# Performance work log

Hardware: AMD Instinct MI355X
Metric: run time of the kernel (lower is better)

## Reference

```python
import jax, jax.numpy as jnp
import numpy as np

N = 50000
NEG_SLOPE = 0.2

def gat_conv(x, src, dst, W, a_src, a_dst, bias, heads, out_ch):
    # Linear projection per head: [N, H, C]
    h = (x @ W).reshape(x.shape[0], heads, out_ch)
    # Node-level attention terms alpha_src/alpha_dst: [N, H]
    al_src = jnp.einsum('nhc,hc->nh', h, a_src)
    al_dst = jnp.einsum('nhc,hc->nh', h, a_dst)
    # Edge logits with LeakyReLU: [E, H]
    logits = jax.nn.leaky_relu(al_src[src] + al_dst[dst], NEG_SLOPE)
    # Segment softmax over incoming edges of each dst node
    m = jax.ops.segment_max(logits, dst, num_segments=N)
    e = jnp.exp(logits - m[dst])
    s = jax.ops.segment_sum(e, dst, num_segments=N)
    alpha = e / (s[dst] + 1e-16)                      # [E, H]
    # Weighted message aggregation (scatter-add): [N, H, C]
    out = jax.ops.segment_sum(h[src] * alpha[..., None], dst, num_segments=N)
    return out.reshape(N, heads * out_ch) + bias


def setup_inputs() -> dict:
    key = jax.random.key(0)
    ks = jax.random.split(key, 12)
    in_ch, out_ch = 128, 256
    h1, c1 = 4, out_ch // 8          # conv1: 4 heads x 32
    mid = h1 * c1                    # 128 = out_ch // 2
    E = 1600000
    x = jax.random.normal(ks[0], (N, in_ch), jnp.float32)
    edge_index = jax.random.randint(ks[1], (2, E), 0, N, jnp.int64)
    sc = 0.1
    return {
        'x': x,
        'edge_index': edge_index,
        'W1': jax.random.normal(ks[2], (in_ch, h1 * c1), jnp.float32) * sc,
        'a_src1': jax.random.normal(ks[3], (h1, c1), jnp.float32) * sc,
        'a_dst1': jax.random.normal(ks[4], (h1, c1), jnp.float32) * sc,
        'b1': jnp.zeros((h1 * c1,), jnp.float32),
        'W2': jax.random.normal(ks[5], (mid, out_ch), jnp.float32) * sc,
        'a_src2': jax.random.normal(ks[6], (1, out_ch), jnp.float32) * sc,
        'a_dst2': jax.random.normal(ks[7], (1, out_ch), jnp.float32) * sc,
        'b2': jnp.zeros((out_ch,), jnp.float32),
    }


def reference(x, edge_index, W1, a_src1, a_dst1, b1, W2, a_src2, a_dst2, b2):
    # PyG GATConv adds self-loops by default
    loop = jnp.arange(N, dtype=edge_index.dtype)
    src = jnp.concatenate([edge_index[0], loop])
    dst = jnp.concatenate([edge_index[1], loop])
    h = gat_conv(x, src, dst, W1, a_src1, a_dst1, b1, heads=4, out_ch=32)
    h = jax.nn.relu(h)
    out = gat_conv(h, src, dst, W2, a_src2, a_dst2, b2, heads=1, out_ch=256)
    return out
```

## Files before the change

### kernel.cpp

```cpp
#include <hip/hip_runtime.h>
#include <hip/hip_fp16.h>
#include <math.h>

#define NSLOPE 0.2f
#define LOG2E  1.44269504f

typedef _Float16 half8 __attribute__((ext_vector_type(8)));
typedef float floatx4 __attribute__((ext_vector_type(4)));
typedef float floatx2 __attribute__((ext_vector_type(2)));

__device__ __forceinline__ float wcalc(float t) {
    float l = fmaxf(t, NSLOPE * t);
    float r;
    asm("v_exp_f32 %0, %1" : "=v"(r) : "v"(l));
    return r;
}

__device__ __forceinline__ void fma_mix8(float* acc, float w, const uint4& v) {
    const unsigned* u = reinterpret_cast<const unsigned*>(&v);
#pragma unroll
    for (int i = 0; i < 4; ++i) {
        asm("v_fma_mix_f32 %0, %1, %2, %0 op_sel:[0,0,0] op_sel_hi:[1,0,0]"
            : "+v"(acc[2 * i]) : "v"(u[i]), "v"(w));
        asm("v_fma_mix_f32 %0, %1, %2, %0 op_sel:[1,0,0] op_sel_hi:[1,0,0]"
            : "+v"(acc[2 * i + 1]) : "v"(u[i]), "v"(w));
    }
}

__device__ __forceinline__ void fma8_fp8(float* acc, float w, uint2 v) {
    floatx2 p0 = __builtin_amdgcn_cvt_pk_f32_fp8(v.x, false);
    floatx2 p1 = __builtin_amdgcn_cvt_pk_f32_fp8(v.x, true);
    floatx2 p2 = __builtin_amdgcn_cvt_pk_f32_fp8(v.y, false);
    floatx2 p3 = __builtin_amdgcn_cvt_pk_f32_fp8(v.y, true);
    acc[0] = fmaf(w, p0.x, acc[0]);
    acc[1] = fmaf(w, p0.y, acc[1]);
    acc[2] = fmaf(w, p1.x, acc[2]);
    acc[3] = fmaf(w, p1.y, acc[3]);
    acc[4] = fmaf(w, p2.x, acc[4]);
    acc[5] = fmaf(w, p2.y, acc[5]);
    acc[6] = fmaf(w, p3.x, acc[6]);
    acc[7] = fmaf(w, p3.y, acc[7]);
}

#define MAXB 5632
#define BE   8192

__global__ __launch_bounds__(256)
void prep_kernel(const int* __restrict__ dst, int* __restrict__ bcnt,
                 const float* __restrict__ x, __half* __restrict__ x16, int nx,
                 const float* __restrict__ W1, __half* __restrict__ W1T,
                 const float* __restrict__ W2, __half* __restrict__ W2T,
                 const float* __restrict__ a_src2, const float* __restrict__ a_dst2,
                 float* __restrict__ w2s, float* __restrict__ w2d,
                 int E, int Etot, int nb, int nbA, int ncast, int nt1, int nt2)
{
    __shared__ int hist[512];
    int bid = blockIdx.x;
    int tid = threadIdx.x;

    if (bid < nbA) {
        for (int i = tid; i < 512; i += 256) hist[i] = 0;
        __syncthreads();
        for (int e = bid * 256 + tid; e < Etot; e += nbA * 256) {
            int d = (e < E) ? dst[e] : (e - E);
            atomicAdd(&hist[d >> 7], 1);
        }
        __syncthreads();
        for (int i = tid; i < nb; i += 256) {
            int v = hist[i];
            if (v) atomicAdd(&bcnt[i], v);
        }
        return;
    }
    bid -= nbA;
    if (bid < ncast) {
        int i = (bid * 256 + tid) * 4;
        if (i < nx) {
            float4 v = *(const float4*)&x[i];
            __half2 a = __floats2half2_rn(v.x, v.y);
            __half2 b = __floats2half2_rn(v.z, v.w);
            *(uint2*)&x16[i] = make_uint2(*(unsigned*)&a, *(unsigned*)&b);
        }
        return;
    }
    bid -= ncast;
    if (bid < nt1) {
        int idx = bid * 256 + tid;
        int c = idx >> 7, k = idx & 127;
        W1T[(size_t)c * 128 + k] = __float2half(W1[(size_t)k * 128 + c]);
        return;
    }
    bid -= nt1;
    if (bid < nt2) {
        int idx = bid * 256 + tid;
        int c = idx >> 7, k = idx & 127;
        W2T[(size_t)c * 128 + k] = __float2half(W2[(size_t)k * 256 + c]);
        return;
    }
    {
        const float* a = (tid < 128) ? a_src2 : a_dst2;
        int k = tid & 127;
        float acc = 0.f;
        for (int c = 0; c < 256; c += 4) {
            float4 w = *(const float4*)&W2[(size_t)k * 256 + c];
            float4 av = *(const float4*)&a[c];
            acc = fmaf(w.x, av.x, fmaf(w.y, av.y, fmaf(w.z, av.z, fmaf(w.w, av.w, acc))));
        }
        if (tid < 128) w2s[k] = acc * LOG2E; else w2d[k] = acc * LOG2E;
    }
}

__global__ __launch_bounds__(512)
void scanBuckets_kernel(const int* __restrict__ bcnt, int* __restrict__ bbase,
                        int* __restrict__ gcur, int nb, int* __restrict__ offs,
                        int N, int total)
{
    __shared__ int tmp[512];
    int tid = threadIdx.x;
    int v = (tid < nb) ? bcnt[tid] : 0;
    tmp[tid] = v;
    __syncthreads();
    for (int off = 1; off < 512; off <<= 1) {
        int t = (tid >= off) ? tmp[tid - off] : 0;
        __syncthreads();
        tmp[tid] += t;
        __syncthreads();
    }
    if (tid < nb) {
        int e = tmp[tid] - v;
        bbase[tid] = e;
        gcur[tid] = e;
    }
    if (tid == 0) offs[N] = total;
}

__global__ __launch_bounds__(256)
void bucketB_kernel(const int* __restrict__ src, const int* __restrict__ dst,
                    int* __restrict__ gcur, unsigned* __restrict__ eout,
                    int E, int Etot, int nb)
{
    __shared__ int hist[512];
    __shared__ int res[512];
    __shared__ int lcur[512];
    int tid = threadIdx.x;
    int e0 = blockIdx.x * BE;
    int e1 = min(e0 + BE, Etot);

    for (int i = tid; i < 512; i += 256) hist[i] = 0;
    __syncthreads();
    for (int e = e0 + tid; e < e1; e += 256) {
        int d = (e < E) ? dst[e] : (e - E);
        atomicAdd(&hist[d >> 7], 1);
    }
    __syncthreads();
    for (int i = tid; i < nb; i += 256) {
        int h = hist[i];
        res[i] = h ? atomicAdd(&gcur[i], h) : 0;
        lcur[i] = 0;
    }
    __syncthreads();
    for (int e = e0 + tid; e < e1; e += 256) {
        int s, d;
        if (e < E) { s = src[e]; d = dst[e]; }
        else       { s = e - E; d = s; }
        int b = d >> 7;
        int p = res[b] + atomicAdd(&lcur[b], 1);
        eout[p] = (unsigned)s | ((unsigned)(d & 127) << 16);
    }
}

__global__ __launch_bounds__(256)
void combo_kernel(const unsigned* __restrict__ eout, const int* __restrict__ bbase,
                  const int* __restrict__ bcnt, unsigned short* __restrict__ csr,
                  int* __restrict__ offs, int N, int nb,
                  const __half* __restrict__ A16, const __half* __restrict__ W1T,
                  const float* __restrict__ a_src, const float* __restrict__ a_dst,
                  unsigned char* __restrict__ h1, float* __restrict__ al_src,
                  float* __restrict__ al_dst)
{
    __shared__ unsigned eb[MAXB];
    __shared__ unsigned short sbuf[MAXB];
    __shared__ int cnt128[128], cur128[128], sc[128];

    int tid = threadIdx.x;
    if ((int)blockIdx.x < nb) {
        int b = blockIdx.x;
        int ebase = bbase[b];
        int ecnt = bcnt[b];
        int n0 = b << 7;
        int ncount = min(128, N - n0);

        if (tid < 128) cnt128[tid] = 0;
        for (int i = tid; i < ecnt; i += 256) eb[i] = eout[ebase + i];
        __syncthreads();
        for (int i = tid; i < ecnt; i += 256) atomicAdd(&cnt128[eb[i] >> 16], 1);
        __syncthreads();
        if (tid < 128) sc[tid] = cnt128[tid];
        __syncthreads();
        for (int off = 1; off < 128; off <<= 1) {
            int t = (tid >= off && tid < 128) ? sc[tid - off] : 0;
            __syncthreads();
            if (tid < 128) sc[tid] += t;
            __syncthreads();
        }
        if (tid < 128) {
            int excl = sc[tid] - cnt128[tid];
            cur128[tid] = excl;
            if (tid < ncount) offs[n0 + tid] = ebase + excl;
        }
        __syncthreads();
        for (int i = tid; i < ecnt; i += 256) {
            unsigned v = eb[i];
            int p = atomicAdd(&cur128[v >> 16], 1);
            sbuf[p] = (unsigned short)(v & 0xFFFFu);
        }
        __syncthreads();
        for (int i = tid; i < ecnt; i += 256) csr[ebase + i] = sbuf[i];
        return;
    }

    int gb = blockIdx.x - nb;
    int M = N;
    int wave = tid >> 6, lane = tid & 63;
    int lr = lane & 15, q = lane >> 4;
    int r0 = gb * 32 + (wave >> 1) * 16;
    int wcol = (wave & 1) * 64;

    int arow = min(r0 + lr, M - 1);
    const uint4* Arow = (const uint4*)A16 + (size_t)arow * 16;
    half8 a[4];
#pragma unroll
    for (int kb = 0; kb < 4; ++kb) {
        union { uint4 u; half8 h; } c;
        c.u = Arow[kb * 4 + q];
        a[kb] = c.h;
    }

    floatx4 acc[4];
    const floatx4 zero = {0.f, 0.f, 0.f, 0.f};
#pragma unroll
    for (int ct = 0; ct < 4; ++ct) acc[ct] = zero;

#pragma unroll
    for (int ct = 0; ct < 4; ++ct) {
        const uint4* Brow = (const uint4*)W1T + (size_t)(wcol + ct * 16 + lr) * 16;
#pragma unroll
        for (int kb = 0; kb < 4; ++kb) {
            union { uint4 u; half8 h; } c;
            c.u = Brow[kb * 4 + q];
            acc[ct] = __builtin_amdgcn_mfma_f32_16x16x32_f16(a[kb], c.h, acc[ct], 0, 0, 0);
        }
    }

#pragma unroll
    for (int ct = 0; ct < 4; ++ct) {
        int col = wcol + ct * 16 + lr;
#pragma unroll
        for (int r = 0; r < 4; ++r) {
            int row = r0 + q * 4 + r;
            if (row < M) {
                unsigned pk = __builtin_amdgcn_cvt_pk_fp8_f32(acc[ct][r], acc[ct][r], 0, false);
                h1[(size_t)row * 128 + col] = (unsigned char)(pk & 0xFF);
            }
        }
    }

    float as[4], ad[4];
#pragma unroll
    for (int ct = 0; ct < 4; ++ct) {
        int col = wcol + ct * 16 + lr;
        as[ct] = a_src[col] * LOG2E;
        ad[ct] = a_dst[col] * LOG2E;
    }
    int hb = wcol >> 5;
#pragma unroll
    for (int r = 0; r < 4; ++r) {
        float psA = acc[0][r] * as[0] + acc[1][r] * as[1];
        float psB = acc[2][r] * as[2] + acc[3][r] * as[3];
        float pdA = acc[0][r] * ad[0] + acc[1][r] * ad[1];
        float pdB = acc[2][r] * ad[2] + acc[3][r] * ad[3];
#pragma unroll
        for (int off = 1; off < 16; off <<= 1) {
            psA += __shfl_xor(psA, off); psB += __shfl_xor(psB, off);
            pdA += __shfl_xor(pdA, off); pdB += __shfl_xor(pdB, off);
        }
        if (lr == 0) {
            int row = r0 + q * 4 + r;
            if (row < M) {
                al_src[(size_t)row * 4 + hb]     = psA;
                al_src[(size_t)row * 4 + hb + 1] = psB;
                al_dst[(size_t)row * 4 + hb]     = pdA;
                al_dst[(size_t)row * 4 + hb + 1] = pdB;
            }
        }
    }
}

__global__ __launch_bounds__(256)
void gemm2_mfma(const __half* __restrict__ A16, const __half* __restrict__ W2T,
                const float* __restrict__ bias, float* __restrict__ out, int M)
{
    int wave = threadIdx.x >> 6, lane = threadIdx.x & 63;
    int lr = lane & 15, q = lane >> 4;
    int r0 = blockIdx.x * 16;
    int c0 = wave * 64;

    int arow = min(r0 + lr, M - 1);
    const uint4* Arow = (const uint4*)A16 + (size_t)arow * 16;
    half8 a[4];
#pragma unroll
    for (int kb = 0; kb < 4; ++kb) {
        union { uint4 u; half8 h; } c;
        c.u = Arow[kb * 4 + q];
        a[kb] = c.h;
    }

    floatx4 acc[4];
    const floatx4 zero = {0.f, 0.f, 0.f, 0.f};
#pragma unroll
    for (int ct = 0; ct < 4; ++ct) acc[ct] = zero;

#pragma unroll
    for (int ct = 0; ct < 4; ++ct) {
        const uint4* Brow = (const uint4*)W2T + (size_t)(c0 + ct * 16 + lr) * 16;
#pragma unroll
        for (int kb = 0; kb < 4; ++kb) {
            union { uint4 u; half8 h; } c;
            c.u = Brow[kb * 4 + q];
            acc[ct] = __builtin_amdgcn_mfma_f32_16x16x32_f16(a[kb], c.h, acc[ct], 0, 0, 0);
        }
    }

#pragma unroll
    for (int ct = 0; ct < 4; ++ct) {
        int col = c0 + ct * 16 + lr;
        float b = bias[col];
#pragma unroll
        for (int r = 0; r < 4; ++r) {
            int row = r0 + q * 4 + r;
            if (row < M) out[(size_t)row * 256 + col] = acc[ct][r] + b;
        }
    }
}

__global__ __launch_bounds__(256)
void agg1_kernel(const unsigned char* __restrict__ feat, const unsigned short* __restrict__ csr_src,
                 const int* __restrict__ offs, const float* __restrict__ alS,
                 const float* __restrict__ alD, const float* __restrict__ bias,
                 const float* __restrict__ w2s, const float* __restrict__ w2d,
                 __half* __restrict__ hmid, float* __restrict__ alS2,
                 float* __restrict__ alD2, int N)
{
    int lane = threadIdx.x & 63;
    int n = blockIdx.x * 4 + (threadIdx.x >> 6);
    if (n >= N) return;

    int lc = lane & 15;
    int es = lane >> 4;
    int h = lc >> 2;

    float aD = alD[(size_t)n * 4 + h];
    int beg = offs[n], end = offs[n + 1];

    float acc0[8] = {0,0,0,0,0,0,0,0}, acc1[8] = {0,0,0,0,0,0,0,0};
    float sw0 = 0.f, sw1 = 0.f;
    const char* fbase = (const char*)feat + lc * 8;
    const float* alSh = alS + h;

    int j = beg + es;
    for (; j + 12 < end; j += 16) {
        int s0 = csr_src[j];
        int s1 = csr_src[j + 4];
        int s2 = csr_src[j + 8];
        int s3 = csr_src[j + 12];
        float w0 = wcalc(alSh[(size_t)s0 * 4] + aD);
        float w1 = wcalc(alSh[(size_t)s1 * 4] + aD);
        float w2 = wcalc(alSh[(size_t)s2 * 4] + aD);
        float w3 = wcalc(alSh[(size_t)s3 * 4] + aD);
        uint2 f0 = *(const uint2*)(fbase + (size_t)s0 * 128);
        uint2 f1 = *(const uint2*)(fbase + (size_t)s1 * 128);
        uint2 f2 = *(const uint2*)(fbase + (size_t)s2 * 128);
        uint2 f3 = *(const uint2*)(fbase + (size_t)s3 * 128);
        fma8_fp8(acc0, w0, f0); sw0 += w0;
        fma8_fp8(acc1, w1, f1); sw1 += w1;
        fma8_fp8(acc0, w2, f2); sw0 += w2;
        fma8_fp8(acc1, w3, f3); sw1 += w3;
    }
    for (; j < end; j += 4) {
        int s0 = csr_src[j];
        float w0 = wcalc(alSh[(size_t)s0 * 4] + aD);
        uint2 f0 = *(const uint2*)(fbase + (size_t)s0 * 128);
        fma8_fp8(acc0, w0, f0); sw0 += w0;
    }

    float sw = sw0 + sw1;
    sw += __shfl_xor(sw, 16); sw += __shfl_xor(sw, 32);
#pragma unroll
    for (int i = 0; i < 8; ++i) {
        acc0[i] += acc1[i];
        acc0[i] += __shfl_xor(acc0[i], 16);
        acc0[i] += __shfl_xor(acc0[i], 32);
    }

    if (lane < 16) {
        float inv = 1.f / (sw + 1e-16f);
        float v[8];
#pragma unroll
        for (int i = 0; i < 8; ++i)
            v[i] = fmaxf(fmaf(acc0[i], inv, bias[lc * 8 + i]), 0.f);
        __half2 p0 = __floats2half2_rn(v[0], v[1]);
        __half2 p1 = __floats2half2_rn(v[2], v[3]);
        __half2 p2 = __floats2half2_rn(v[4], v[5]);
        __half2 p3 = __floats2half2_rn(v[6], v[7]);
        uint4 pk = make_uint4(*(unsigned*)&p0, *(unsigned*)&p1,
                              *(unsigned*)&p2, *(unsigned*)&p3);
        ((uint4*)hmid)[(size_t)n * 16 + lc] = pk;
        float ps = 0.f, pd = 0.f;
#pragma unroll
        for (int i = 0; i < 8; ++i) {
            ps = fmaf(v[i], w2s[lc * 8 + i], ps);
            pd = fmaf(v[i], w2d[lc * 8 + i], pd);
        }
        ps += __shfl_xor(ps, 1); ps += __shfl_xor(ps, 2);
        ps += __shfl_xor(ps, 4); ps += __shfl_xor(ps, 8);
        pd += __shfl_xor(pd, 1); pd += __shfl_xor(pd, 2);
        pd += __shfl_xor(pd, 4); pd += __shfl_xor(pd, 8);
        if (lane == 0) { alS2[n] = ps; alD2[n] = pd; }
    }
}

__global__ __launch_bounds__(256)
void agg2_kernel(const __half* __restrict__ feat, const unsigned short* __restrict__ csr_src,
                 const int* __restrict__ offs, const float* __restrict__ alS,
                 const float* __restrict__ alD, __half* __restrict__ m16, int N)
{
    int lane = threadIdx.x & 63;
    int n = blockIdx.x * 4 + (threadIdx.x >> 6);
    if (n >= N) return;

    int lc = lane & 15;
    int es = lane >> 4;

    float aD = alD[n];
    int beg = offs[n], end = offs[n + 1];

    float acc0[8] = {0,0,0,0,0,0,0,0}, acc1[8] = {0,0,0,0,0,0,0,0};
    float sw0 = 0.f, sw1 = 0.f;
    const char* fbase = (const char*)feat + lc * 16;

    int j = beg + es;
    for (; j + 12 < end; j += 16) {
        int s0 = csr_src[j];
        int s1 = csr_src[j + 4];
        int s2 = csr_src[j + 8];
        int s3 = csr_src[j + 12];
        float w0 = wcalc(alS[s0] + aD);
        float w1 = wcalc(alS[s1] + aD);
        float w2 = wcalc(alS[s2] + aD);
        float w3 = wcalc(alS[s3] + aD);
        uint4 f0 = *(const uint4*)(fbase + (size_t)s0 * 256);
        uint4 f1 = *(const uint4*)(fbase + (size_t)s1 * 256);
        uint4 f2 = *(const uint4*)(fbase + (size_t)s2 * 256);
        uint4 f3 = *(const uint4*)(fbase + (size_t)s3 * 256);
        fma_mix8(acc0, w0, f0); sw0 += w0;
        fma_mix8(acc1, w1, f1); sw1 += w1;
        fma_mix8(acc0, w2, f2); sw0 += w2;
        fma_mix8(acc1, w3, f3); sw1 += w3;
    }
    for (; j < end; j += 4) {
        int s0 = csr_src[j];
        float w0 = wcalc(alS[s0] + aD);
        uint4 f0 = *(const uint4*)(fbase + (size_t)s0 * 256);
        fma_mix8(acc0, w0, f0); sw0 += w0;
    }

    float sw = sw0 + sw1;
    sw += __shfl_xor(sw, 16); sw += __shfl_xor(sw, 32);
#pragma unroll
    for (int i = 0; i < 8; ++i) {
        acc0[i] += acc1[i];
        acc0[i] += __shfl_xor(acc0[i], 16);
        acc0[i] += __shfl_xor(acc0[i], 32);
    }

    if (lane < 16) {
        float inv = 1.f / (sw + 1e-16f);
        float v[8];
#pragma unroll
        for (int i = 0; i < 8; ++i) v[i] = acc0[i] * inv;
        __half2 p0 = __floats2half2_rn(v[0], v[1]);
        __half2 p1 = __floats2half2_rn(v[2], v[3]);
        __half2 p2 = __floats2half2_rn(v[4], v[5]);
        __half2 p3 = __floats2half2_rn(v[6], v[7]);
        uint4 pk = make_uint4(*(unsigned*)&p0, *(unsigned*)&p1,
                              *(unsigned*)&p2, *(unsigned*)&p3);
        ((uint4*)m16)[(size_t)n * 16 + lc] = pk;
    }
}

extern "C" void kernel_launch(void* const* d_in, const int* in_sizes, int n_in,
                              void* d_out, int out_size, void* d_ws, size_t ws_size,
                              hipStream_t stream)
{
    const float* x      = (const float*)d_in[0];
    const int*   ei     = (const int*)d_in[1];
    const float* W1     = (const float*)d_in[2];
    const float* a_src1 = (const float*)d_in[3];
    const float* a_dst1 = (const float*)d_in[4];
    const float* b1     = (const float*)d_in[5];
    const float* W2     = (const float*)d_in[6];
    const float* a_src2 = (const float*)d_in[7];
    const float* a_dst2 = (const float*)d_in[8];
    const float* b2     = (const float*)d_in[9];

    const int N    = in_sizes[0] / 128;
    const int E    = in_sizes[1] / 2;
    const int Etot = E + N;
    const int* src = ei;
    const int* dst = ei + E;
    const int nb   = (N + 127) >> 7;

    char* ws = (char*)d_ws;
    size_t off = 0;
    auto carve = [&](size_t bytes) -> void* {
        void* p = ws + off;
        off += (bytes + 255) & ~(size_t)255;
        return p;
    };
    __half*  x16  = (__half*)carve((size_t)N * 128 * 2);
    unsigned char* h1 = (unsigned char*)carve((size_t)N * 128);
    __half*  hmid = (__half*)carve((size_t)N * 128 * 2);
    __half*  m16  = (__half*)carve((size_t)N * 128 * 2);
    __half*  W1T  = (__half*)carve(128 * 128 * 2);
    __half*  W2T  = (__half*)carve(256 * 128 * 2);
    float*   alS1 = (float*)carve((size_t)N * 4 * 4);
    float*   alD1 = (float*)carve((size_t)N * 4 * 4);
    float*   alS2 = (float*)carve((size_t)N * 4);
    float*   alD2 = (float*)carve((size_t)N * 4);
    float*   w2s  = (float*)carve(128 * 4);
    float*   w2d  = (float*)carve(128 * 4);
    int*     offs = (int*)carve((size_t)(N + 1) * 4);
    int*     bcnt = (int*)carve(512 * 4);
    int*     bbas = (int*)carve(512 * 4);
    int*     gcur = (int*)carve(512 * 4);
    unsigned* eout = (unsigned*)carve((size_t)Etot * 4);
    unsigned short* csr = (unsigned short*)carve((size_t)Etot * 2);
    (void)ws_size; (void)n_in; (void)out_size;

    const int TB = 256;
    const int agrid = (N + 3) / 4;
    const int g1grid = (N + 31) / 32;
    const int g2grid = (N + 15) / 16;
    const int nx = N * 128;

    const int nbA   = 512;
    const int ncast = (nx / 4 + TB - 1) / TB;
    const int nt1   = (128 * 128 + TB - 1) / TB;
    const int nt2   = (256 * 128 + TB - 1) / TB;
    const int nprep = nbA + ncast + nt1 + nt2 + 1;

    hipMemsetAsync(bcnt, 0, 512 * 4, stream);

    prep_kernel<<<nprep, TB, 0, stream>>>(dst, bcnt, x, x16, nx, W1, W1T, W2, W2T,
                                          a_src2, a_dst2, w2s, w2d,
                                          E, Etot, nb, nbA, ncast, nt1, nt2);
    scanBuckets_kernel<<<1, 512, 0, stream>>>(bcnt, bbas, gcur, nb, offs, N, Etot);
    bucketB_kernel<<<(Etot + BE - 1) / BE, TB, 0, stream>>>(src, dst, gcur, eout, E, Etot, nb);
    combo_kernel<<<nb + g1grid, TB, 0, stream>>>(eout, bbas, bcnt, csr, offs, N, nb,
                                                 x16, W1T, a_src1, a_dst1, h1, alS1, alD1);
    agg1_kernel<<<agrid, TB, 0, stream>>>(h1, csr, offs, alS1, alD1, b1,
                                          w2s, w2d, hmid, alS2, alD2, N);
    agg2_kernel<<<agrid, TB, 0, stream>>>(hmid, csr, offs, alS2, alD2, m16, N);
    gemm2_mfma<<<g2grid, TB, 0, stream>>>(m16, W2T, b2, (float*)d_out, N);
}
```

Baseline: 299.7 us.

## Split feature aggregation into column halves with fp8 intermediates for cache locality

```diff
diff --git a/kernel.cpp b/kernel.cpp
--- a/kernel.cpp
+++ b/kernel.cpp
@@ -14,17 +14,6 @@
     float r;
     asm("v_exp_f32 %0, %1" : "=v"(r) : "v"(l));
     return r;
-}
-
-__device__ __forceinline__ void fma_mix8(float* acc, float w, const uint4& v) {
-    const unsigned* u = reinterpret_cast<const unsigned*>(&v);
-#pragma unroll
-    for (int i = 0; i < 4; ++i) {
-        asm("v_fma_mix_f32 %0, %1, %2, %0 op_sel:[0,0,0] op_sel_hi:[1,0,0]"
-            : "+v"(acc[2 * i]) : "v"(u[i]), "v"(w));
-        asm("v_fma_mix_f32 %0, %1, %2, %0 op_sel:[1,0,0] op_sel_hi:[1,0,0]"
-            : "+v"(acc[2 * i + 1]) : "v"(u[i]), "v"(w));
-    }
 }
 
 __device__ __forceinline__ void fma8_fp8(float* acc, float w, uint2 v) {
@@ -175,8 +164,8 @@
                   int* __restrict__ offs, int N, int nb,
                   const __half* __restrict__ A16, const __half* __restrict__ W1T,
                   const float* __restrict__ a_src, const float* __restrict__ a_dst,
-                  unsigned char* __restrict__ h1, float* __restrict__ al_src,
-                  float* __restrict__ al_dst)
+                  unsigned char* __restrict__ h1A, unsigned char* __restrict__ h1B,
+                  float* __restrict__ al_src, float* __restrict__ al_dst)
 {
     __shared__ unsigned eb[MAXB];
     __shared__ unsigned short sbuf[MAXB];
@@ -225,6 +214,7 @@
     int lr = lane & 15, q = lane >> 4;
     int r0 = gb * 32 + (wave >> 1) * 16;
     int wcol = (wave & 1) * 64;
+    unsigned char* hT = (wave & 1) ? h1B : h1A;
 
     int arow = min(r0 + lr, M - 1);
     const uint4* Arow = (const uint4*)A16 + (size_t)arow * 16;
@@ -254,13 +244,13 @@
 
 #pragma unroll
     for (int ct = 0; ct < 4; ++ct) {
-        int col = wcol + ct * 16 + lr;
+        int colh = ct * 16 + lr;
 #pragma unroll
         for (int r = 0; r < 4; ++r) {
             int row = r0 + q * 4 + r;
             if (row < M) {
                 unsigned pk = __builtin_amdgcn_cvt_pk_fp8_f32(acc[ct][r], acc[ct][r], 0, false);
-                h1[(size_t)row * 128 + col] = (unsigned char)(pk & 0xFF);
+                hT[(size_t)row * 64 + colh] = (unsigned char)(pk & 0xFF);
             }
         }
     }
@@ -344,146 +334,135 @@
 }
 
 __global__ __launch_bounds__(256)
-void agg1_kernel(const unsigned char* __restrict__ feat, const unsigned short* __restrict__ csr_src,
-                 const int* __restrict__ offs, const float* __restrict__ alS,
-                 const float* __restrict__ alD, const float* __restrict__ bias,
-                 const float* __restrict__ w2s, const float* __restrict__ w2d,
-                 __half* __restrict__ hmid, float* __restrict__ alS2,
-                 float* __restrict__ alD2, int N)
+void agg1_half_kernel(const unsigned char* __restrict__ feat,
+                      const unsigned short* __restrict__ csr_src,
+                      const int* __restrict__ offs, const float* __restrict__ alS,
+                      const float* __restrict__ alD, const float* __restrict__ bias,
+                      const float* __restrict__ w2s, const float* __restrict__ w2d,
+                      unsigned char* __restrict__ hmidH, float* __restrict__ alS2,
+                      float* __restrict__ alD2, int N, int half)
 {
     int lane = threadIdx.x & 63;
     int n = blockIdx.x * 4 + (threadIdx.x >> 6);
     if (n >= N) return;
 
-    int lc = lane & 15;
-    int es = lane >> 4;
-    int h = lc >> 2;
-
-    float aD = alD[(size_t)n * 4 + h];
+    int lc = lane & 7;
+    int es = lane >> 3;
+    int head = half * 2 + (lc >> 2);
+
+    float aD = alD[(size_t)n * 4 + head];
     int beg = offs[n], end = offs[n + 1];
 
     float acc0[8] = {0,0,0,0,0,0,0,0}, acc1[8] = {0,0,0,0,0,0,0,0};
     float sw0 = 0.f, sw1 = 0.f;
     const char* fbase = (const char*)feat + lc * 8;
-    const float* alSh = alS + h;
+    const float* alSh = alS + head;
 
     int j = beg + es;
-    for (; j + 12 < end; j += 16) {
+    for (; j + 8 < end; j += 16) {
         int s0 = csr_src[j];
-        int s1 = csr_src[j + 4];
-        int s2 = csr_src[j + 8];
-        int s3 = csr_src[j + 12];
+        int s1 = csr_src[j + 8];
         float w0 = wcalc(alSh[(size_t)s0 * 4] + aD);
         float w1 = wcalc(alSh[(size_t)s1 * 4] + aD);
-        float w2 = wcalc(alSh[(size_t)s2 * 4] + aD);
-        float w3 = wcalc(alSh[(size_t)s3 * 4] + aD);
-        uint2 f0 = *(const uint2*)(fbase + (size_t)s0 * 128);
-        uint2 f1 = *(const uint2*)(fbase + (size_t)s1 * 128);
-        uint2 f2 = *(const uint2*)(fbase + (size_t)s2 * 128);
-        uint2 f3 = *(const uint2*)(fbase + (size_t)s3 * 128);
+        uint2 f0 = *(const uint2*)(fbase + (size_t)s0 * 64);
+        uint2 f1 = *(const uint2*)(fbase + (size_t)s1 * 64);
         fma8_fp8(acc0, w0, f0); sw0 += w0;
         fma8_fp8(acc1, w1, f1); sw1 += w1;
-        fma8_fp8(acc0, w2, f2); sw0 += w2;
-        fma8_fp8(acc1, w3, f3); sw1 += w3;
-    }
-    for (; j < end; j += 4) {
+    }
+    if (j < end) {
         int s0 = csr_src[j];
         float w0 = wcalc(alSh[(size_t)s0 * 4] + aD);
-        uint2 f0 = *(const uint2*)(fbase + (size_t)s0 * 128);
+        uint2 f0 = *(const uint2*)(fbase + (size_t)s0 * 64);
         fma8_fp8(acc0, w0, f0); sw0 += w0;
     }
 
     float sw = sw0 + sw1;
-    sw += __shfl_xor(sw, 16); sw += __shfl_xor(sw, 32);
+    sw += __shfl_xor(sw, 8); sw += __shfl_xor(sw, 16); sw += __shfl_xor(sw, 32);
 #pragma unroll
     for (int i = 0; i < 8; ++i) {
         acc0[i] += acc1[i];
+        acc0[i] += __shfl_xor(acc0[i], 8);
         acc0[i] += __shfl_xor(acc0[i], 16);
         acc0[i] += __shfl_xor(acc0[i], 32);
     }
 
-    if (lane < 16) {
+    if (lane < 8) {
         float inv = 1.f / (sw + 1e-16f);
+        int cb = half * 64 + lc * 8;
         float v[8];
 #pragma unroll
         for (int i = 0; i < 8; ++i)
-            v[i] = fmaxf(fmaf(acc0[i], inv, bias[lc * 8 + i]), 0.f);
-        __half2 p0 = __floats2half2_rn(v[0], v[1]);
-        __half2 p1 = __floats2half2_rn(v[2], v[3]);
-        __half2 p2 = __floats2half2_rn(v[4], v[5]);
-        __half2 p3 = __floats2half2_rn(v[6], v[7]);
-        uint4 pk = make_uint4(*(unsigned*)&p0, *(unsigned*)&p1,
-                              *(unsigned*)&p2, *(unsigned*)&p3);
-        ((uint4*)hmid)[(size_t)n * 16 + lc] = pk;
+            v[i] = fmaxf(fmaf(acc0[i], inv, bias[cb + i]), 0.f);
+        unsigned pk0 = __builtin_amdgcn_cvt_pk_fp8_f32(v[0], v[1], 0, false);
+        pk0 = __builtin_amdgcn_cvt_pk_fp8_f32(v[2], v[3], pk0, true);
+        unsigned pk1 = __builtin_amdgcn_cvt_pk_fp8_f32(v[4], v[5], 0, false);
+        pk1 = __builtin_amdgcn_cvt_pk_fp8_f32(v[6], v[7], pk1, true);
+        ((uint2*)hmidH)[(size_t)n * 8 + lc] = make_uint2(pk0, pk1);
         float ps = 0.f, pd = 0.f;
 #pragma unroll
         for (int i = 0; i < 8; ++i) {
-            ps = fmaf(v[i], w2s[lc * 8 + i], ps);
-            pd = fmaf(v[i], w2d[lc * 8 + i], pd);
-        }
-        ps += __shfl_xor(ps, 1); ps += __shfl_xor(ps, 2);
-        ps += __shfl_xor(ps, 4); ps += __shfl_xor(ps, 8);
-        pd += __shfl_xor(pd, 1); pd += __shfl_xor(pd, 2);
-        pd += __shfl_xor(pd, 4); pd += __shfl_xor(pd, 8);
-        if (lane == 0) { alS2[n] = ps; alD2[n] = pd; }
+            ps = fmaf(v[i], w2s[cb + i], ps);
+            pd = fmaf(v[i], w2d[cb + i], pd);
+        }
+        ps += __shfl_xor(ps, 1); ps += __shfl_xor(ps, 2); ps += __shfl_xor(ps, 4);
+        pd += __shfl_xor(pd, 1); pd += __shfl_xor(pd, 2); pd += __shfl_xor(pd, 4);
+        if (lane == 0) {
+            if (half == 0) { alS2[n] = ps;          alD2[n] = pd; }
+            else           { alS2[n] = alS2[n] + ps; alD2[n] = alD2[n] + pd; }
+        }
     }
 }
 
 __global__ __launch_bounds__(256)
-void agg2_kernel(const __half* __restrict__ feat, const unsigned short* __restrict__ csr_src,
-                 const int* __restrict__ offs, const float* __restrict__ alS,
-                 const float* __restrict__ alD, __half* __restrict__ m16, int N)
+void agg2_half_kernel(const unsigned char* __restrict__ feat,
+                      const unsigned short* __restrict__ csr_src,
+                      const int* __restrict__ offs, const float* __restrict__ alS,
+                      const float* __restrict__ alD, __half* __restrict__ m16,
+                      int N, int half)
 {
     int lane = threadIdx.x & 63;
     int n = blockIdx.x * 4 + (threadIdx.x >> 6);
     if (n >= N) return;
 
-    int lc = lane & 15;
-    int es = lane >> 4;
+    int lc = lane & 7;
+    int es = lane >> 3;
 
     float aD = alD[n];
     int beg = offs[n], end = offs[n + 1];
 
     float acc0[8] = {0,0,0,0,0,0,0,0}, acc1[8] = {0,0,0,0,0,0,0,0};
     float sw0 = 0.f, sw1 = 0.f;
-    const char* fbase = (const char*)feat + lc * 16;
+    const char* fbase = (const char*)feat + lc * 8;
 
     int j = beg + es;
-    for (; j + 12 < end; j += 16) {
+    for (; j + 8 < end; j += 16) {
         int s0 = csr_src[j];
-        int s1 = csr_src[j + 4];
-        int s2 = csr_src[j + 8];
-        int s3 = csr_src[j + 12];
+        int s1 = csr_src[j + 8];
         float w0 = wcalc(alS[s0] + aD);
         float w1 = wcalc(alS[s1] + aD);
-        float w2 = wcalc(alS[s2] + aD);
-        float w3 = wcalc(alS[s3] + aD);
-        uint4 f0 = *(const uint4*)(fbase + (size_t)s0 * 256);
-        uint4 f1 = *(const uint4*)(fbase + (size_t)s1 * 256);
-        uint4 f2 = *(const uint4*)(fbase + (size_t)s2 * 256);
-        uint4 f3 = *(const uint4*)(fbase + (size_t)s3 * 256);
-        fma_mix8(acc0, w0, f0); sw0 += w0;
-        fma_mix8(acc1, w1, f1); sw1 += w1;
-        fma_mix8(acc0, w2, f2); sw0 += w2;
-        fma_mix8(acc1, w3, f3); sw1 += w3;
-    }
-    for (; j < end; j += 4) {
+        uint2 f0 = *(const uint2*)(fbase + (size_t)s0 * 64);
+        uint2 f1 = *(const uint2*)(fbase + (size_t)s1 * 64);
+        fma8_fp8(acc0, w0, f0); sw0 += w0;
+        fma8_fp8(acc1, w1, f1); sw1 += w1;
+    }
+    if (j < end) {
         int s0 = csr_src[j];
         float w0 = wcalc(alS[s0] + aD);
-        uint4 f0 = *(const uint4*)(fbase + (size_t)s0 * 256);
-        fma_mix8(acc0, w0, f0); sw0 += w0;
+        uint2 f0 = *(const uint2*)(fbase + (size_t)s0 * 64);
+        fma8_fp8(acc0, w0, f0); sw0 += w0;
     }
 
     float sw = sw0 + sw1;
-    sw += __shfl_xor(sw, 16); sw += __shfl_xor(sw, 32);
+    sw += __shfl_xor(sw, 8); sw += __shfl_xor(sw, 16); sw += __shfl_xor(sw, 32);
 #pragma unroll
     for (int i = 0; i < 8; ++i) {
         acc0[i] += acc1[i];
+        acc0[i] += __shfl_xor(acc0[i], 8);
         acc0[i] += __shfl_xor(acc0[i], 16);
         acc0[i] += __shfl_xor(acc0[i], 32);
     }
 
-    if (lane < 16) {
+    if (lane < 8) {
         float inv = 1.f / (sw + 1e-16f);
         float v[8];
 #pragma unroll
@@ -494,7 +473,7 @@
         __half2 p3 = __floats2half2_rn(v[6], v[7]);
         uint4 pk = make_uint4(*(unsigned*)&p0, *(unsigned*)&p1,
                               *(unsigned*)&p2, *(unsigned*)&p3);
-        ((uint4*)m16)[(size_t)n * 16 + lc] = pk;
+        ((uint4*)m16)[(size_t)n * 16 + half * 8 + lc] = pk;
     }
 }
 
@@ -528,8 +507,10 @@
         return p;
     };
     __half*  x16  = (__half*)carve((size_t)N * 128 * 2);
-    unsigned char* h1 = (unsigned char*)carve((size_t)N * 128);
-    __half*  hmid = (__half*)carve((size_t)N * 128 * 2);
+    unsigned char* h1A   = (unsigned char*)carve((size_t)N * 64);
+    unsigned char* h1B   = (unsigned char*)carve((size_t)N * 64);
+    unsigned char* hmidA = (unsigned char*)carve((size_t)N * 64);
+    unsigned char* hmidB = (unsigned char*)carve((size_t)N * 64);
     __half*  m16  = (__half*)carve((size_t)N * 128 * 2);
     __half*  W1T  = (__half*)carve(128 * 128 * 2);
     __half*  W2T  = (__half*)carve(256 * 128 * 2);
@@ -567,9 +548,12 @@
     scanBuckets_kernel<<<1, 512, 0, stream>>>(bcnt, bbas, gcur, nb, offs, N, Etot);
     bucketB_kernel<<<(Etot + BE - 1) / BE, TB, 0, stream>>>(src, dst, gcur, eout, E, Etot, nb);
     combo_kernel<<<nb + g1grid, TB, 0, stream>>>(eout, bbas, bcnt, csr, offs, N, nb,
-                                                 x16, W1T, a_src1, a_dst1, h1, alS1, alD1);
-    agg1_kernel<<<agrid, TB, 0, stream>>>(h1, csr, offs, alS1, alD1, b1,
-                                          w2s, w2d, hmid, alS2, alD2, N);
-    agg2_kernel<<<agrid, TB, 0, stream>>>(hmid, csr, offs, alS2, alD2, m16, N);
+                                                 x16, W1T, a_src1, a_dst1, h1A, h1B, alS1, alD1);
+    agg1_half_kernel<<<agrid, TB, 0, stream>>>(h1A, csr, offs, alS1, alD1, b1,
+                                               w2s, w2d, hmidA, alS2, alD2, N, 0);
+    agg1_half_kernel<<<agrid, TB, 0, stream>>>(h1B, csr, offs, alS1, alD1, b1,
+                                               w2s, w2d, hmidB, alS2, alD2, N, 1);
+    agg2_half_kernel<<<agrid, TB, 0, stream>>>(hmidA, csr, offs, alS2, alD2, m16, N, 0);
+    agg2_half_kernel<<<agrid, TB, 0, stream>>>(hmidB, csr, offs, alS2, alD2, m16, N, 1);
     gemm2_mfma<<<g2grid, TB, 0, stream>>>(m16, W2T, b2, (float*)d_out, N);
 }
```

After: 336.8 us. 12.4% more time.
